# Kernel optimization log

Measured on AMD Instinct MI355X. Metric: run time of the kernel, lower is better.

The kernel has to match this reference:

```python
import jax, jax.numpy as jnp
import numpy as np
from jax import lax

N = 2048
B = 8
CH = 10
START = 1
STOP = 65


def setup_inputs() -> dict:
    key = jax.random.key(0)
    ks = jax.random.split(key, 13)

    def g(k, s):
        return jax.random.normal(k, s, jnp.float32) * 0.05

    return {
        "x": jax.random.normal(ks[0], (B, 1, N, N), jnp.float32),
        "wl": g(ks[1], (CH // 2, 1, 3, N)), "bl": g(ks[2], (CH // 2,)),
        "wr": g(ks[3], (CH // 2, 1, N, 3)), "br": g(ks[4], (CH // 2,)),
        "wA": g(ks[5], (CH, CH, 3)), "bA": g(ks[6], (CH,)),
        "wB": g(ks[7], (CH, CH, 3)), "bB": g(ks[8], (CH,)),  # shared by layers 2&3 (torch list aliasing)
        "wT": g(ks[9], (CH, CH, 3)), "bT": g(ks[10], (CH,)),
        "wm": g(ks[11], (2, CH, 1)), "bm": g(ks[12], (2,)),
        "start": START, "stop": STOP,
    }


def _conv1d(h, w, b, pad):
    y = lax.conv_general_dilated(h, w, (1,), [(pad, pad)], dimension_numbers=("NCH", "OIH", "NCH"))
    return y + b[None, :, None]


def _forward(x, wl, bl, wr, br, wA, bA, wB, bB, wT, bT, wm, bm, start, stop):
    n = x.shape[-1]
    # scan_left: Conv2d kernel (3, n), padding (1, 0) -> (B, 5, n, 1) -> squeeze
    left_ = lax.conv_general_dilated(x, wl, (1, 1), [(1, 1), (0, 0)], dimension_numbers=("NCHW", "OIHW", "NCHW"))
    left_ = left_[..., 0] + bl[None, :, None]
    # scan_right: Conv2d kernel (n, 3), padding (0, 1) -> (B, 5, 1, n) -> squeeze
    right_ = lax.conv_general_dilated(x, wr, (1, 1), [(0, 0), (1, 1)], dimension_numbers=("NCHW", "OIHW", "NCHW"))
    right_ = right_[:, :, 0, :] + br[None, :, None]
    lr = jnp.concatenate([left_, right_], axis=1)  # (B, 10, n)
    h = jax.nn.relu(_conv1d(lr, wA, bA, 1))
    h = jax.nn.relu(_conv1d(h, wB, bB, 1))  # same weights twice: torch [conv, relu]*2 aliasing
    h = jax.nn.relu(_conv1d(h, wB, bB, 1))
    # ConvTranspose1d(k=3, stride=1, pad=1) == Conv1d with transposed, spatially-flipped kernel, pad=1
    wTc = jnp.flip(jnp.swapaxes(wT, 0, 1), -1)
    for _ in range(3):
        h = jax.nn.relu(_conv1d(h, wTc, bT, 1))
    m = jax.nn.sigmoid(_conv1d(h, wm, bm, 0))  # (B, 2, n)
    left, right = m[:, 0, :], m[:, 1, :]
    xs = x[:, 0]  # (B, n, n)
    preds = []
    for d in range(start, stop):  # static diagonal indices
        curr = jnp.exp(jnp.diagonal(xs, offset=d, axis1=1, axis2=2))  # (B, n-d)
        mass_in = curr[:, 1:] * right[:, 1:n - d] + curr[:, :-1] * left[:, d:n - 1]
        mass_out = right[:, 0:n - d - 1] + left[:, d + 1:n]
        p = jnp.log(mass_in / mass_out)
        preds.append(p - jnp.mean(p))  # scalar mean over batch+positions, as torch.mean
    return jnp.concatenate(preds, axis=1)  # ragged preds concatenated: (B, sum(n-d-1))


def reference(x, wl, bl, wr, br, wA, bA, wB, bB, wT, bT, wm, bm, start, stop):
    return _forward(x, wl, bl, wr, br, wA, bA, wB, bB, wT, bT, wm, bm, start, stop)
```

## Files before the change

### kernel.cpp

```cpp
#include <hip/hip_runtime.h>
#include <hip/hip_bf16.h>

#define NN 2048
#define BB 8
#define TROW 128928

__global__ __launch_bounds__(256) void k_left(const float* __restrict__ x,
                                              const float* __restrict__ wl,
                                              const float* __restrict__ wr,
                                              float* __restrict__ R,
                                              float* __restrict__ WF,
                                              float* __restrict__ psum) {
    if (blockIdx.x == 0 && threadIdx.x < 64) psum[threadIdx.x] = 0.f;
    if (blockIdx.x < 128) {
        int idx = blockIdx.x * 256 + threadIdx.x;
        int h = idx >> 4, k = idx & 15;
        float v = 0.f;
        if (k < 15) {
            int c = k / 3, dw = k - c * 3;
            v = wr[c * (NN * 3) + h * 3 + dw];
        }
        WF[idx] = v;
    }
    __shared__ float red[4][30 * 65];
    int b = blockIdx.x >> 8;
    int rg = blockIdx.x & 255;
    int wv = threadIdx.x >> 6, lane = threadIdx.x & 63;
    int r0 = rg * 8 + wv * 2;
    const float* xp = x + ((size_t)(b * NN + r0)) * NN;

    float acc[2][15];
#pragma unroll
    for (int r = 0; r < 2; r++)
#pragma unroll
        for (int k = 0; k < 15; k++) acc[r][k] = 0.f;

    for (int seg = 0; seg < 8; seg++) {
        int j0 = seg * 256 + lane * 4;
        float4 xv[2];
#pragma unroll
        for (int r = 0; r < 2; r++) xv[r] = *(const float4*)(xp + (size_t)r * NN + j0);
#pragma unroll
        for (int k = 0; k < 15; k++) {
            float4 w4 = *(const float4*)(wl + (size_t)k * NN + j0);
#pragma unroll
            for (int r = 0; r < 2; r++) {
                acc[r][k] = fmaf(xv[r].x, w4.x, acc[r][k]);
                acc[r][k] = fmaf(xv[r].y, w4.y, acc[r][k]);
                acc[r][k] = fmaf(xv[r].z, w4.z, acc[r][k]);
                acc[r][k] = fmaf(xv[r].w, w4.w, acc[r][k]);
            }
        }
    }
#pragma unroll
    for (int r = 0; r < 2; r++)
#pragma unroll
        for (int k = 0; k < 15; k++) red[wv][(r * 15 + k) * 65 + lane] = acc[r][k];
    __syncthreads();
    if (lane < 30) {
        const float* rp = &red[wv][lane * 65];
        float s = 0.f;
#pragma unroll
        for (int j = 0; j < 64; j++) s += rp[j];
        int r = lane / 15, k = lane - r * 15;
        R[(size_t)(b * NN + r0 + r) * 16 + k] = s;
    }
}

__global__ __launch_bounds__(512) void k_right(const float* __restrict__ x,
                                               const float* __restrict__ WF,
                                               float* __restrict__ CSp) {
    int b = blockIdx.x >> 5;
    int rem = blockIdx.x & 31;
    int jc = rem >> 4, rc = rem & 15;
    int r0 = rc * 128;
    int w = threadIdx.x >> 6, lane = threadIdx.x & 63;
    int c0 = jc * 1024 + w * 128 + lane * 2;
    const float* xp = x + ((size_t)b * NN + r0) * NN + c0;

    float acc[15][2];
#pragma unroll
    for (int k = 0; k < 15; k++) { acc[k][0] = 0.f; acc[k][1] = 0.f; }

    for (int rb = 0; rb < 16; rb++) {
        float2 xv[8];
#pragma unroll
        for (int q = 0; q < 8; q++)
            xv[q] = *(const float2*)(xp + (size_t)(rb * 8 + q) * NN);
#pragma unroll
        for (int q = 0; q < 8; q++) {
            const float* wrow = WF + (size_t)(r0 + rb * 8 + q) * 16;
#pragma unroll
            for (int k = 0; k < 15; k++) {
                float wk = wrow[k];
                acc[k][0] = fmaf(xv[q].x, wk, acc[k][0]);
                acc[k][1] = fmaf(xv[q].y, wk, acc[k][1]);
            }
        }
    }
    float* outp = CSp + ((size_t)(rc * BB + b) * 16) * NN + c0;
#pragma unroll
    for (int k = 0; k < 15; k++) {
        float2 v; v.x = acc[k][0]; v.y = acc[k][1];
        *(float2*)(outp + (size_t)k * NN) = v;
    }
}

__global__ __launch_bounds__(256) void k_csum(const float* __restrict__ CSp,
                                              float* __restrict__ CS) {
    int vid = blockIdx.x * 256 + threadIdx.x;
    const float4* src = (const float4*)CSp;
    float4 s = src[vid];
#pragma unroll
    for (int rc = 1; rc < 16; rc++) {
        float4 v = src[vid + rc * 65536];
        s.x += v.x; s.y += v.y; s.z += v.z; s.w += v.w;
    }
    ((float4*)CS)[vid] = s;
}

__global__ __launch_bounds__(256) void k_chainC(const float* __restrict__ R,
                                                const float* __restrict__ CS,
                                                const float* __restrict__ bl,
                                                const float* __restrict__ br,
                                                const float* __restrict__ wA, const float* __restrict__ bA,
                                                const float* __restrict__ wB, const float* __restrict__ bB,
                                                const float* __restrict__ wT, const float* __restrict__ bT,
                                                const float* __restrict__ wm, const float* __restrict__ bm,
                                                float* __restrict__ LEFT, float* __restrict__ RIGHT) {
    __shared__ float buf0[10][144], buf1[10][144];
    __shared__ float W[3][10][10][3];
    __shared__ float Bs[3][10];
    __shared__ float Wm[2][10], Bm[2];
    int b = blockIdx.x >> 4;
    int c0 = (blockIdx.x & 15) << 7;
    int tid = threadIdx.x;

    for (int idx = tid; idx < 900; idx += 256) {
        int set = idx / 300, rem = idx - set * 300;
        int o = rem / 30, rem2 = rem - o * 30, c = rem2 / 3, kk = rem2 - c * 3;
        float u;
        if (set == 0) u = wA[o * 30 + c * 3 + kk];
        else if (set == 1) u = wB[o * 30 + c * 3 + kk];
        else u = wT[c * 30 + o * 3 + (2 - kk)];
        W[set][o][c][kk] = u;
    }
    if (tid < 30) {
        float v = (tid < 10) ? bA[tid] : (tid < 20) ? bB[tid - 10] : bT[tid - 20];
        Bs[tid / 10][tid % 10] = v;
    }
    if (tid < 20) Wm[tid / 10][tid % 10] = wm[tid];
    if (tid < 2) Bm[tid] = bm[tid];

    for (int idx = tid; idx < 1400; idx += 256) {
        int ch = idx / 140, p = idx - ch * 140;
        int g = c0 - 6 + p;
        float v = 0.f;
        if (g >= 0 && g < NN) {
            if (ch < 5) {
                v = bl[ch];
#pragma unroll
                for (int dh = 0; dh < 3; dh++) {
                    int r = g + dh - 1;
                    if (r >= 0 && r < NN) v += R[(size_t)(b * NN + r) * 16 + ch * 3 + dh];
                }
            } else {
                int c = ch - 5;
                v = br[c];
#pragma unroll
                for (int dw = 0; dw < 3; dw++) {
                    int j = g + dw - 1;
                    if (j >= 0 && j < NN)
                        v += CS[((size_t)b * 16 + c * 3 + dw) * NN + j];
                }
            }
        }
        buf0[ch][p] = v;
    }
    __syncthreads();

    float(*in)[144] = buf0;
    float(*out)[144] = buf1;
    for (int layer = 0; layer < 6; layer++) {
        int set = (layer == 0) ? 0 : (layer < 3 ? 1 : 2);
        int lo = layer + 1;
        for (int idx = tid; idx < 1400; idx += 256) {
            int o = idx / 140, p = idx - o * 140;
            if (p >= lo && p < 140 - lo) {
                float s = Bs[set][o];
#pragma unroll
                for (int c = 0; c < 10; c++) {
                    const float* ip = &in[c][p];
                    s = fmaf(ip[-1], W[set][o][c][0], s);
                    s = fmaf(ip[0], W[set][o][c][1], s);
                    s = fmaf(ip[1], W[set][o][c][2], s);
                }
                s = s > 0.f ? s : 0.f;
                int g = c0 - 6 + p;
                if (g < 0 || g >= NN) s = 0.f;
                out[o][p] = s;
            }
        }
        __syncthreads();
        float(*tmp)[144] = in; in = out; out = tmp;
    }
    {
        int idx = tid;
        int o = idx >> 7, pp = idx & 127;
        int p = 6 + pp;
        float s = Bm[o];
#pragma unroll
        for (int c = 0; c < 10; c++) s = fmaf(in[c][p], Wm[o][c], s);
        float sig = 1.f / (1.f + __expf(-s));
        (o ? RIGHT : LEFT)[b * NN + c0 + pp] = sig;
    }
}

__global__ __launch_bounds__(256) void k_diagmass(const float* __restrict__ x,
                                                  const float* __restrict__ LEFT,
                                                  const float* __restrict__ RIGHT,
                                                  float* __restrict__ P,
                                                  float* __restrict__ psum) {
    __shared__ float T[65][65];
    __shared__ float psl[64];
    int b = blockIdx.x >> 5;
    int i0 = (blockIdx.x & 31) << 6;
    int tid = threadIdx.x;

    for (int idx = tid; idx < 65 * 64; idx += 256) {
        int r = idx >> 6, dm1 = idx & 63;
        int row = i0 + r;
        int col = row + dm1 + 1;
        float v = 0.f;
        if (row < NN && col < NN) v = __expf(x[((size_t)b * NN + row) * NN + col]);
        T[r][dm1] = v;
    }
    __syncthreads();

    int wv = tid >> 6, lane = tid & 63;
    int i = i0 + lane;
    const float* lf = LEFT + b * NN;
    const float* rt = RIGHT + b * NN;
#pragma unroll
    for (int s = 0; s < 16; s++) {
        int dm1 = wv * 16 + s;
        int d = dm1 + 1;
        int L = (NN - 1) - d;
        float p = 0.f;
        if (i < L) {
            float mi = T[lane + 1][dm1] * rt[i + 1] + T[lane][dm1] * lf[d + i];
            float mo = rt[i] + lf[d + 1 + i];
            p = __logf(mi / mo);
            P[((size_t)dm1 * BB + b) * NN + i] = p;
        }
        float s64 = p;
        for (int off = 32; off; off >>= 1) s64 += __shfl_down(s64, off);
        if (lane == 0) psl[dm1] = s64;
    }
    __syncthreads();
    if (tid < 64) atomicAdd(&psum[tid], psl[tid]);
}

__global__ __launch_bounds__(1024) void k_out(const float* __restrict__ P,
                                              const float* __restrict__ psum,
                                              float* __restrict__ outp) {
    int dm1 = blockIdx.x >> 2, q = blockIdx.x & 3;
    int d = dm1 + 1;
    int L = (NN - 1) - d;
    int tid = threadIdx.x;
    int b2 = tid >> 9, ii = tid & 511;
    int i = q * 512 + ii;
    if (i >= L) return;
    float mean = psum[dm1] / (float)(8 * L);
    size_t off0 = (size_t)dm1 * (NN - 1) - (size_t)dm1 * (dm1 + 1) / 2;
#pragma unroll
    for (int bs = 0; bs < 4; bs++) {
        int b = b2 + bs * 2;
        outp[(size_t)b * TROW + off0 + i] = P[((size_t)dm1 * BB + b) * NN + i] - mean;
    }
}

extern "C" void kernel_launch(void* const* d_in, const int* in_sizes, int n_in,
                              void* d_out, int out_size, void* d_ws, size_t ws_size,
                              hipStream_t stream) {
    const float* x = (const float*)d_in[0];
    const float* wl = (const float*)d_in[1];
    const float* bl = (const float*)d_in[2];
    const float* wr = (const float*)d_in[3];
    const float* br = (const float*)d_in[4];
    const float* wA = (const float*)d_in[5];
    const float* bA = (const float*)d_in[6];
    const float* wB = (const float*)d_in[7];
    const float* bB = (const float*)d_in[8];
    const float* wT = (const float*)d_in[9];
    const float* bT = (const float*)d_in[10];
    const float* wm = (const float*)d_in[11];
    const float* bm = (const float*)d_in[12];

    float* ws = (float*)d_ws;
    float* R    = ws;
    float* CSp  = ws + 262144;
    float* WF   = ws + 4456448;
    float* CS   = ws + 4489216;
    float* LEFT = ws + 4751360;
    float* RIGHT= ws + 4767744;
    float* P    = ws + 4784128;
    float* psum = ws + 5832704;

    k_left<<<2048, 256, 0, stream>>>(x, wl, wr, R, WF, psum);
    k_right<<<256, 512, 0, stream>>>(x, WF, CSp);
    k_csum<<<256, 256, 0, stream>>>(CSp, CS);
    k_chainC<<<128, 256, 0, stream>>>(R, CS, bl, br, wA, bA, wB, bB, wT, bT, wm, bm, LEFT, RIGHT);
    k_diagmass<<<256, 256, 0, stream>>>(x, LEFT, RIGHT, P, psum);
    k_out<<<256, 1024, 0, stream>>>(P, psum, (float*)d_out);
}
```

Measured before the change: 329.6 us.

## Compute left-scan conv with bf16 MFMA and split-K partial sums

Replaces the FP32 FMA dot-product kernel for the left scan (x rows times wl) with a bf16 MFMA 16x16x32 kernel. It converts fp32 inputs to bf16 in registers and splits K into four chunks whose partials are summed in the existing csum kernel. The goal is to move this GEMV-like work onto matrix cores and drop the shared-memory reduction. In exchange, bf16 rounding of x and the weights lowers precision, and the split-K partials add extra workspace traffic.

```diff
diff --git a/kernel.cpp b/kernel.cpp
--- a/kernel.cpp
+++ b/kernel.cpp
@@ -5,12 +5,21 @@
 #define BB 8
 #define TROW 128928
 
-__global__ __launch_bounds__(256) void k_left(const float* __restrict__ x,
-                                              const float* __restrict__ wl,
-                                              const float* __restrict__ wr,
-                                              float* __restrict__ R,
-                                              float* __restrict__ WF,
-                                              float* __restrict__ psum) {
+typedef __attribute__((ext_vector_type(8))) short bf16x8;
+typedef __attribute__((ext_vector_type(4))) float f32x4;
+
+__device__ __forceinline__ short f2bf(float f) {
+    unsigned u = __float_as_uint(f);
+    unsigned r = (u + 0x7FFFu + ((u >> 16) & 1u)) >> 16;
+    return (short)r;
+}
+
+__global__ __launch_bounds__(256) void k_leftm(const float* __restrict__ x,
+                                               const float* __restrict__ wl,
+                                               const float* __restrict__ wr,
+                                               float* __restrict__ Rp,
+                                               float* __restrict__ WF,
+                                               float* __restrict__ psum) {
     if (blockIdx.x == 0 && threadIdx.x < 64) psum[threadIdx.x] = 0.f;
     if (blockIdx.x < 128) {
         int idx = blockIdx.x * 256 + threadIdx.x;
@@ -22,49 +31,38 @@
         }
         WF[idx] = v;
     }
-    __shared__ float red[4][30 * 65];
-    int b = blockIdx.x >> 8;
-    int rg = blockIdx.x & 255;
+    int b = blockIdx.x >> 7;
+    int sub = blockIdx.x & 127;
+    int rg = sub >> 2, ks = sub & 3;
     int wv = threadIdx.x >> 6, lane = threadIdx.x & 63;
-    int r0 = rg * 8 + wv * 2;
-    const float* xp = x + ((size_t)(b * NN + r0)) * NN;
-
-    float acc[2][15];
-#pragma unroll
-    for (int r = 0; r < 2; r++)
-#pragma unroll
-        for (int k = 0; k < 15; k++) acc[r][k] = 0.f;
-
-    for (int seg = 0; seg < 8; seg++) {
-        int j0 = seg * 256 + lane * 4;
-        float4 xv[2];
-#pragma unroll
-        for (int r = 0; r < 2; r++) xv[r] = *(const float4*)(xp + (size_t)r * NN + j0);
-#pragma unroll
-        for (int k = 0; k < 15; k++) {
-            float4 w4 = *(const float4*)(wl + (size_t)k * NN + j0);
-#pragma unroll
-            for (int r = 0; r < 2; r++) {
-                acc[r][k] = fmaf(xv[r].x, w4.x, acc[r][k]);
-                acc[r][k] = fmaf(xv[r].y, w4.y, acc[r][k]);
-                acc[r][k] = fmaf(xv[r].z, w4.z, acc[r][k]);
-                acc[r][k] = fmaf(xv[r].w, w4.w, acc[r][k]);
-            }
-        }
-    }
-#pragma unroll
-    for (int r = 0; r < 2; r++)
-#pragma unroll
-        for (int k = 0; k < 15; k++) red[wv][(r * 15 + k) * 65 + lane] = acc[r][k];
-    __syncthreads();
-    if (lane < 30) {
-        const float* rp = &red[wv][lane * 65];
-        float s = 0.f;
-#pragma unroll
-        for (int j = 0; j < 64; j++) s += rp[j];
-        int r = lane / 15, k = lane - r * 15;
-        R[(size_t)(b * NN + r0 + r) * 16 + k] = s;
-    }
+    int q = lane >> 4, m = lane & 15;
+    int r0 = rg * 64 + wv * 16;
+    int nrow = (m == 15) ? 14 : m;
+    int k0 = ks * 512 + q * 8;
+
+    const float* ap = x + ((size_t)(b * NN + r0 + m)) * NN + k0;
+    const float* bp = wl + (size_t)nrow * NN + k0;
+
+    f32x4 acc = {0.f, 0.f, 0.f, 0.f};
+#pragma unroll 4
+    for (int it = 0; it < 16; it++) {
+        const float* a0 = ap + it * 32;
+        const float* b0 = bp + it * 32;
+        float4 av0 = *(const float4*)(a0);
+        float4 av1 = *(const float4*)(a0 + 4);
+        float4 bv0 = *(const float4*)(b0);
+        float4 bv1 = *(const float4*)(b0 + 4);
+        bf16x8 af, bf;
+        af[0] = f2bf(av0.x); af[1] = f2bf(av0.y); af[2] = f2bf(av0.z); af[3] = f2bf(av0.w);
+        af[4] = f2bf(av1.x); af[5] = f2bf(av1.y); af[6] = f2bf(av1.z); af[7] = f2bf(av1.w);
+        bf[0] = f2bf(bv0.x); bf[1] = f2bf(bv0.y); bf[2] = f2bf(bv0.z); bf[3] = f2bf(bv0.w);
+        bf[4] = f2bf(bv1.x); bf[5] = f2bf(bv1.y); bf[6] = f2bf(bv1.z); bf[7] = f2bf(bv1.w);
+        acc = __builtin_amdgcn_mfma_f32_16x16x32_bf16(af, bf, acc, 0, 0, 0);
+    }
+    float* rp = Rp + (size_t)ks * 262144 + ((size_t)b * NN + r0) * 16;
+#pragma unroll
+    for (int reg = 0; reg < 4; reg++)
+        rp[(q * 4 + reg) * 16 + m] = acc[reg];
 }
 
 __global__ __launch_bounds__(512) void k_right(const float* __restrict__ x,
@@ -107,16 +105,31 @@
 }
 
 __global__ __launch_bounds__(256) void k_csum(const float* __restrict__ CSp,
-                                              float* __restrict__ CS) {
-    int vid = blockIdx.x * 256 + threadIdx.x;
-    const float4* src = (const float4*)CSp;
-    float4 s = src[vid];
-#pragma unroll
-    for (int rc = 1; rc < 16; rc++) {
-        float4 v = src[vid + rc * 65536];
-        s.x += v.x; s.y += v.y; s.z += v.z; s.w += v.w;
-    }
-    ((float4*)CS)[vid] = s;
+                                              float* __restrict__ CS,
+                                              const float* __restrict__ Rp,
+                                              float* __restrict__ R) {
+    int blk = blockIdx.x;
+    if (blk < 256) {
+        int vid = blk * 256 + threadIdx.x;
+        const float4* src = (const float4*)CSp;
+        float4 s = src[vid];
+#pragma unroll
+        for (int rc = 1; rc < 16; rc++) {
+            float4 v = src[vid + rc * 65536];
+            s.x += v.x; s.y += v.y; s.z += v.z; s.w += v.w;
+        }
+        ((float4*)CS)[vid] = s;
+    } else {
+        int vid = (blk - 256) * 256 + threadIdx.x;
+        const float4* src = (const float4*)Rp;
+        float4 s = src[vid];
+#pragma unroll
+        for (int ks = 1; ks < 4; ks++) {
+            float4 v = src[vid + ks * 65536];
+            s.x += v.x; s.y += v.y; s.z += v.z; s.w += v.w;
+        }
+        ((float4*)R)[vid] = s;
+    }
 }
 
 __global__ __launch_bounds__(256) void k_chainC(const float* __restrict__ R,
@@ -299,17 +312,18 @@
 
     float* ws = (float*)d_ws;
     float* R    = ws;
-    float* CSp  = ws + 262144;
-    float* WF   = ws + 4456448;
-    float* CS   = ws + 4489216;
-    float* LEFT = ws + 4751360;
-    float* RIGHT= ws + 4767744;
-    float* P    = ws + 4784128;
-    float* psum = ws + 5832704;
-
-    k_left<<<2048, 256, 0, stream>>>(x, wl, wr, R, WF, psum);
+    float* Rp   = ws + 262144;
+    float* CSp  = ws + 1310720;
+    float* WF   = ws + 5505024;
+    float* CS   = ws + 5537792;
+    float* LEFT = ws + 5799936;
+    float* RIGHT= ws + 5816320;
+    float* P    = ws + 5832704;
+    float* psum = ws + 6881280;
+
+    k_leftm<<<1024, 256, 0, stream>>>(x, wl, wr, Rp, WF, psum);
     k_right<<<256, 512, 0, stream>>>(x, WF, CSp);
-    k_csum<<<256, 256, 0, stream>>>(CSp, CS);
+    k_csum<<<512, 256, 0, stream>>>(CSp, CS, Rp, R);
     k_chainC<<<128, 256, 0, stream>>>(R, CS, bl, br, wA, bA, wB, bB, wT, bT, wm, bm, LEFT, RIGHT);
     k_diagmass<<<256, 256, 0, stream>>>(x, LEFT, RIGHT, P, psum);
     k_out<<<256, 1024, 0, stream>>>(P, psum, (float*)d_out);
```

Measured after the change: 305.9 us. -7.2%, faster.
